# Optimization experiments

Hardware: AMD Instinct MI355X
Metric: run time of the kernel (lower is better)

Reference implementation:

```python
import jax, jax.numpy as jnp
import numpy as np

B, N, D = 32, 4096, 256      # batch, num input features, input dim
S, H, M = 11, 256, 512       # num_slots, slot_size, mlp_hidden_size
ITERS = 3
ATTN_EPS = 1e-8
LN_EPS = 1e-5


def layer_norm(x, scale, offset):
    mu = jnp.mean(x, axis=-1, keepdims=True)
    var = jnp.var(x, axis=-1, keepdims=True)
    return (x - mu) * scale * jax.lax.rsqrt(var + LN_EPS) + offset


def gru_unroll(updates, w_i, w_h, b):
    # haiku hk.GRU unrolled over axis 1 (time_major=False), zero initial state.
    # updates: [B, T, H]
    h0 = jnp.zeros((updates.shape[0], H), updates.dtype)
    def step(h, x):
        gx = jnp.matmul(x, w_i)                                    # [B, 3H]
        zr = jax.nn.sigmoid(gx[:, :2 * H] + jnp.matmul(h, w_h[:, :2 * H]) + b[:2 * H])
        z, r = zr[:, :H], zr[:, H:]
        a = jnp.tanh(gx[:, 2 * H:] + jnp.matmul(r * h, w_h[:, 2 * H:]) + b[2 * H:])
        h_new = (1.0 - z) * h + z * a
        return h_new, h_new
    _, outs = jax.lax.scan(step, h0, jnp.swapaxes(updates, 0, 1))
    return jnp.swapaxes(outs, 0, 1)                                # [B, T, H]


def setup_inputs():
    key = jax.random.key(0)
    k = jax.random.split(key, 16)
    def lin(kk, fan_in, fan_out):
        return jax.random.normal(kk, (fan_in, fan_out), jnp.float32) / np.sqrt(fan_in).astype(np.float32)
    return {
        "inputs": jax.random.normal(k[0], (B, N, D), jnp.float32),
        "slot_noise": jax.random.normal(k[1], (B, S, H), jnp.float32),
        "ln_in_scale": jnp.ones((D,), jnp.float32),
        "ln_in_offset": jnp.zeros((D,), jnp.float32),
        "ln_slots_scale": jnp.ones((H,), jnp.float32),
        "ln_slots_offset": jnp.zeros((H,), jnp.float32),
        "ln_mlp_scale": jnp.ones((H,), jnp.float32),
        "ln_mlp_offset": jnp.zeros((H,), jnp.float32),
        "slots_mu": jax.random.normal(k[2], (1, 1, H), jnp.float32) * 0.1,
        "slots_log_sigma": jax.random.normal(k[3], (1, 1, H), jnp.float32) * 0.1 - 1.0,
        "Wq": lin(k[4], H, H),
        "Wk": lin(k[5], D, H),
        "Wv": lin(k[6], D, H),
        "gru_wi": lin(k[7], H, 3 * H),
        "gru_wh": lin(k[8], H, 3 * H),
        "gru_b": jnp.zeros((3 * H,), jnp.float32),
        "mlp_w1": lin(k[9], H, M),
        "mlp_b1": jnp.zeros((M,), jnp.float32),
        "mlp_w2": lin(k[10], M, H),
        "mlp_b2": jnp.zeros((H,), jnp.float32),
    }


def reference(inputs, slot_noise, ln_in_scale, ln_in_offset, ln_slots_scale,
              ln_slots_offset, ln_mlp_scale, ln_mlp_offset, slots_mu,
              slots_log_sigma, Wq, Wk, Wv, gru_wi, gru_wh, gru_b,
              mlp_w1, mlp_b1, mlp_w2, mlp_b2):
    x = layer_norm(inputs, ln_in_scale, ln_in_offset)
    kf = jnp.matmul(x, Wk)                                          # [B, N, H]
    vf = jnp.matmul(x, Wv)                                          # [B, N, H]
    slots = slots_mu + jnp.exp(slots_log_sigma) * slot_noise        # [B, S, H]
    scale = H ** (-0.5)
    for _ in range(ITERS):
        q = jnp.matmul(layer_norm(slots, ln_slots_scale, ln_slots_offset), Wq) * scale
        attn_logits = jnp.einsum('bnh,bsh->bns', kf, q)             # [B, N, S]
        attn = jax.nn.softmax(attn_logits, axis=-1) + ATTN_EPS      # softmax over slots
        attn = attn / jnp.sum(attn, axis=-2, keepdims=True)         # normalize over inputs
        updates = jnp.einsum('bns,bnh->bsh', attn, vf)              # [B, S, H]
        slots = gru_unroll(updates, gru_wi, gru_wh, gru_b)          # GRU over slot axis
        mlp_in = layer_norm(slots, ln_mlp_scale, ln_mlp_offset)
        hid = jax.nn.relu(jnp.matmul(mlp_in, mlp_w1) + mlp_b1)
        slots = slots + jnp.matmul(hid, mlp_w2) + mlp_b2
    return slots
```

## Files before the change

### kernel.cpp

```cpp
#include <hip/hip_runtime.h>

typedef unsigned short u16;
typedef __bf16 bf16x8 __attribute__((ext_vector_type(8)));
typedef float  f32x4  __attribute__((ext_vector_type(4)));
typedef unsigned short u16x8 __attribute__((ext_vector_type(8)));

union U8cast { u16x8 u; bf16x8 b; };

#define NB 32
#define NN 4096
#define ND 256
#define NS 11
#define NH 256
#define NM 512

__device__ __forceinline__ u16 f2bf(float f) {
  unsigned u = __float_as_uint(f);
  u += 0x7FFF + ((u >> 16) & 1);
  return (u16)(u >> 16);
}
__device__ __forceinline__ float bf2f(u16 h) {
  return __uint_as_float(((unsigned)h) << 16);
}

__global__ void k_stats_ln(const float* __restrict__ x, const float* __restrict__ sc,
                           const float* __restrict__ of, u16* __restrict__ xbf) {
  int lane = threadIdx.x & 63;
  int wid  = threadIdx.x >> 6;
  int row  = blockIdx.x * 4 + wid;
  float4 v = *(const float4*)(x + (size_t)row * 256 + lane * 4);
  float s1 = v.x + v.y + v.z + v.w;
  float s2 = v.x*v.x + v.y*v.y + v.z*v.z + v.w*v.w;
#pragma unroll
  for (int off = 32; off; off >>= 1) { s1 += __shfl_xor(s1, off); s2 += __shfl_xor(s2, off); }
  float mu = s1 * (1.f/256.f);
  float rs = rsqrtf(s2 * (1.f/256.f) - mu*mu + 1e-5f);
  float4 s4 = *(const float4*)(sc + lane * 4);
  float4 o4 = *(const float4*)(of + lane * 4);
  ushort4 o;
  o.x = f2bf((v.x - mu) * (rs * s4.x) + o4.x);
  o.y = f2bf((v.y - mu) * (rs * s4.y) + o4.y);
  o.z = f2bf((v.z - mu) * (rs * s4.z) + o4.z);
  o.w = f2bf((v.w - mu) * (rs * s4.w) + o4.w);
  *(ushort4*)(xbf + (size_t)row * 256 + lane * 4) = o;
}

__global__ __launch_bounds__(256)
void k_cvt_w(const float* __restrict__ Wk, u16* __restrict__ wT) {
  __shared__ float Lt[64][65];
  int bx = blockIdx.x;
  int kt = bx & 3, ct = bx >> 2;
  int k0 = kt * 64, c0 = ct * 64;
  int t = threadIdx.x;
  int kr = t >> 2, part = t & 3;
  const float* sp = Wk + (size_t)(k0 + kr) * 256 + c0 + part * 16;
#pragma unroll
  for (int g = 0; g < 4; ++g) {
    float4 v = *(const float4*)(sp + g * 4);
    Lt[kr][part*16 + g*4 + 0] = v.x;
    Lt[kr][part*16 + g*4 + 1] = v.y;
    Lt[kr][part*16 + g*4 + 2] = v.z;
    Lt[kr][part*16 + g*4 + 3] = v.w;
  }
  __syncthreads();
  int cr = t >> 2;
  u16* wp = wT + (size_t)(c0 + cr) * 256 + k0 + part * 16;
#pragma unroll
  for (int g = 0; g < 2; ++g) {
    u16x8 o;
#pragma unroll
    for (int j = 0; j < 8; ++j) o[j] = f2bf(Lt[part*16 + g*8 + j][cr]);
    *(u16x8*)(wp + g * 8) = o;
  }
}

__global__ __launch_bounds__(256)
void k_mk(const float* __restrict__ Wq, const u16* __restrict__ wT,
          u16* __restrict__ Mb) {
  __shared__ float xn[256];
  __shared__ float part[8][256];
  int e = blockIdx.x, t = threadIdx.x;
  xn[t] = Wq[e*256 + t];
  __syncthreads();
  int tc = t & 31, kg = t >> 5;
  float a[8] = {};
#pragma unroll 8
  for (int kk = 0; kk < 32; ++kk) {
    int k = kg*32 + kk;
    float xv = xn[k];
    u16x8 wv = *(const u16x8*)(wT + k*256 + tc*8);
#pragma unroll
    for (int j = 0; j < 8; ++j) a[j] += xv * bf2f(wv[j]);
  }
  *(float4*)&part[kg][tc*8]     = make_float4(a[0], a[1], a[2], a[3]);
  *(float4*)&part[kg][tc*8 + 4] = make_float4(a[4], a[5], a[6], a[7]);
  __syncthreads();
  float s = 0.f;
#pragma unroll
  for (int g = 0; g < 8; ++g) s += part[g][t];
  Mb[e*256 + t] = f2bf(s);
}

__global__ __launch_bounds__(384)
void k_wvi(const float* __restrict__ Wv, const float* __restrict__ wi,
           u16* __restrict__ wvib) {
  __shared__ float xn[256];
  __shared__ float part[4][768];
  int d = blockIdx.x, t = threadIdx.x;
  if (t < 256) xn[t] = Wv[d*256 + t];
  __syncthreads();
  int tc = t % 96, kg = t / 96;
  float a[8] = {};
#pragma unroll 4
  for (int kk = 0; kk < 64; ++kk) {
    int k = kg*64 + kk;
    float xv = xn[k];
    float4 w0 = *(const float4*)(wi + (size_t)k*768 + tc*8);
    float4 w1 = *(const float4*)(wi + (size_t)k*768 + tc*8 + 4);
    a[0] += xv * w0.x; a[1] += xv * w0.y; a[2] += xv * w0.z; a[3] += xv * w0.w;
    a[4] += xv * w1.x; a[5] += xv * w1.y; a[6] += xv * w1.z; a[7] += xv * w1.w;
  }
  *(float4*)&part[kg][tc*8]     = make_float4(a[0], a[1], a[2], a[3]);
  *(float4*)&part[kg][tc*8 + 4] = make_float4(a[4], a[5], a[6], a[7]);
  __syncthreads();
#pragma unroll
  for (int c = t; c < 768; c += 384) {
    float s = part[0][c] + part[1][c] + part[2][c] + part[3][c];
    wvib[d*768 + c] = f2bf(s);
  }
}

__global__ void k_cvt_all(const float* __restrict__ wh, const float* __restrict__ w1,
                          const float* __restrict__ w2,
                          const float* __restrict__ noise, const float* __restrict__ smu,
                          const float* __restrict__ sls,
                          u16* __restrict__ whb, u16* __restrict__ w1b,
                          u16* __restrict__ w2b, float* __restrict__ slots) {
  int idx = blockIdx.x * 256 + threadIdx.x;
  if      (idx < 196608) whb[idx]          = f2bf(wh[idx]);
  else if (idx < 327680) w1b[idx - 196608] = f2bf(w1[idx - 196608]);
  else if (idx < 458752) w2b[idx - 327680] = f2bf(w2[idx - 327680]);
  else {
    int i = idx - 458752;
    int c = i & 255;
    slots[i] = smu[c] + expf(sls[c]) * noise[i];
  }
}

__global__ __launch_bounds__(256)
void k_q_ln(const float* __restrict__ slots, const float* __restrict__ sc,
            const float* __restrict__ of, const u16* __restrict__ Mb,
            float* __restrict__ qk2, float* __restrict__ updates,
            float* __restrict__ colsum) {
  __shared__ float xn[256];
  __shared__ float red[8];
  __shared__ float part[8][256];
  int row = blockIdx.x, t = threadIdx.x;
  float v = slots[row*256 + t];
  float s1 = v, s2 = v*v;
#pragma unroll
  for (int off = 32; off; off >>= 1) { s1 += __shfl_xor(s1, off); s2 += __shfl_xor(s2, off); }
  int w = t >> 6;
  if ((t & 63) == 0) { red[w*2] = s1; red[w*2+1] = s2; }
  __syncthreads();
  float a1 = red[0] + red[2] + red[4] + red[6];
  float a2 = red[1] + red[3] + red[5] + red[7];
  float mu = a1 * (1.f/256.f);
  float rs = rsqrtf(a2 * (1.f/256.f) - mu*mu + 1e-5f);
  xn[t] = (v - mu) * rs * sc[t] + of[t];
  updates[row*256 + t] = 0.f;
  if (t == 0) colsum[(row/11)*16 + (row%11)] = 0.f;
  __syncthreads();
  int tc = t & 31, kg = t >> 5;
  float a[8] = {};
#pragma unroll 8
  for (int kk = 0; kk < 32; ++kk) {
    int k = kg*32 + kk;
    float xv = xn[k];
    u16x8 wv = *(const u16x8*)(Mb + k*256 + tc*8);
#pragma unroll
    for (int j = 0; j < 8; ++j) a[j] += xv * bf2f(wv[j]);
  }
  *(float4*)&part[kg][tc*8]     = make_float4(a[0], a[1], a[2], a[3]);
  *(float4*)&part[kg][tc*8 + 4] = make_float4(a[4], a[5], a[6], a[7]);
  __syncthreads();
  float s = 0.f;
#pragma unroll
  for (int g = 0; g < 8; ++g) s += part[g][t];
  qk2[row*256 + t] = s * 0.0625f;
}

__global__ __launch_bounds__(256)
void k_attn_up(const u16* __restrict__ xbf, const float* __restrict__ qg,
               float* __restrict__ updates, float* __restrict__ colsum) {
  __shared__ __align__(16) u16 kfL[64][264];
  __shared__ __align__(16) u16 vfL[64][256];
  __shared__ __align__(16) u16 qTL[16][264];
  __shared__ __align__(16) u16 PTL[16][72];
  __shared__ float Lg[64][17];
  int t = threadIdx.x;
  int b = blockIdx.y;
  int nb0 = blockIdx.x * 256;
  int lane = t & 63, w = t >> 6;
  int fr = lane & 15, kq = lane >> 4;

#pragma unroll
  for (int i = t; i < 512; i += 256) {
    int s = i >> 5, k0 = (i & 31) * 8;
    u16x8 o;
    if (s < 11) {
      const float* qp = qg + (size_t)b*2816 + s*256 + k0;
#pragma unroll
      for (int j = 0; j < 8; ++j) o[j] = f2bf(qp[j]);
    } else {
#pragma unroll
      for (int j = 0; j < 8; ++j) o[j] = 0;
    }
    *(u16x8*)&qTL[s][k0] = o;
  }
  for (int i = t; i < 16*72; i += 256) ((u16*)PTL)[i] = 0;

  f32x4 accU[4] = {};
  float cs0 = 0.f, cs1 = 0.f, cs2 = 0.f;
  int rS = t >> 2, g4 = t & 3;

  for (int c = 0; c < 4; ++c) {
    int n0 = nb0 + c*64;
    __syncthreads();
    {
      int hc = (t & 31) * 8;
#pragma unroll
      for (int nr = 0; nr < 8; ++nr) {
        int n = nr*8 + (t >> 5);
        size_t base = ((size_t)b*4096 + n0 + n) * 256;
        u16x8 kvk = *(const u16x8*)(xbf + base + hc);
        *(u16x8*)&kfL[n][hc] = kvk;
        *(u16x8*)&vfL[n][hc ^ (((n >> 3) & 3) * 16)] = kvk;
      }
    }
    __syncthreads();
    {
      f32x4 aL = {};
#pragma unroll
      for (int kc = 0; kc < 256; kc += 32) {
        bf16x8 af = *(const bf16x8*)&kfL[w*16 + fr][kc + kq*8];
        bf16x8 bq = *(const bf16x8*)&qTL[fr][kc + kq*8];
        aL = __builtin_amdgcn_mfma_f32_16x16x32_bf16(af, bq, aL, 0, 0, 0);
      }
#pragma unroll
      for (int r = 0; r < 4; ++r)
        Lg[w*16 + kq*4 + r][fr] = aL[r];
    }
    __syncthreads();
    {
      float p0 = Lg[rS][g4];
      float p1 = Lg[rS][g4 + 4];
      float p2 = (g4 < 3) ? Lg[rS][g4 + 8] : -1e30f;
      float m = fmaxf(fmaxf(p0, p1), p2);
      m = fmaxf(m, __shfl_xor(m, 1));
      m = fmaxf(m, __shfl_xor(m, 2));
      p0 = __expf(p0 - m); p1 = __expf(p1 - m);
      p2 = (g4 < 3) ? __expf(p2 - m) : 0.f;
      float Z = p0 + p1 + p2;
      Z += __shfl_xor(Z, 1);
      Z += __shfl_xor(Z, 2);
      float iz = 1.f / Z;
      u16 b0 = f2bf(p0*iz + 1e-8f);
      u16 b1 = f2bf(p1*iz + 1e-8f);
      PTL[g4][rS]     = b0;  cs0 += bf2f(b0);
      PTL[g4 + 4][rS] = b1;  cs1 += bf2f(b1);
      if (g4 < 3) {
        u16 b2 = f2bf(p2*iz + 1e-8f);
        PTL[g4 + 8][rS] = b2;  cs2 += bf2f(b2);
      }
    }
    __syncthreads();
#pragma unroll
    for (int ht = 0; ht < 4; ++ht) {
      int h = w*64 + ht*16 + fr;
#pragma unroll
      for (int kc = 0; kc < 64; kc += 32) {
        bf16x8 aP = *(const bf16x8*)&PTL[fr][kc + kq*8];
        U8cast bv;
#pragma unroll
        for (int j = 0; j < 8; ++j) {
          int k = kc + kq*8 + j;
          bv.u[j] = vfL[k][h ^ (((k >> 3) & 3) * 16)];
        }
        accU[ht] = __builtin_amdgcn_mfma_f32_16x16x32_bf16(aP, bv.b, accU[ht], 0, 0, 0);
      }
    }
  }
#pragma unroll
  for (int ht = 0; ht < 4; ++ht) {
    int h = w*64 + ht*16 + fr;
#pragma unroll
    for (int r = 0; r < 4; ++r) {
      int s = kq*4 + r;
      if (s < 11)
        atomicAdd(&updates[((size_t)b*11 + s)*256 + h], accU[ht][r]);
    }
  }
  {
#pragma unroll
    for (int off = 4; off < 64; off <<= 1) {
      cs0 += __shfl_xor(cs0, off);
      cs1 += __shfl_xor(cs1, off);
      cs2 += __shfl_xor(cs2, off);
    }
    if (lane < 4) {
      atomicAdd(&colsum[b*16 + lane],     cs0);
      atomicAdd(&colsum[b*16 + lane + 4], cs1);
      if (lane < 3) atomicAdd(&colsum[b*16 + lane + 8], cs2);
    }
  }
}

__global__ __launch_bounds__(384)
void k_gx(const float* __restrict__ updates, const float* __restrict__ colsum,
          const u16* __restrict__ wvib, float* __restrict__ gx) {
  __shared__ float xn[256];
  __shared__ float part[4][768];
  int row = blockIdx.x, t = threadIdx.x;
  if (t < 256) {
    float inv = 1.f / colsum[(row/11)*16 + (row%11)];
    xn[t] = updates[row*256 + t] * inv;
  }
  __syncthreads();
  int tc = t % 96, kg = t / 96;
  float a[8] = {};
#pragma unroll 4
  for (int kk = 0; kk < 64; ++kk) {
    int k = kg*64 + kk;
    float xv = xn[k];
    u16x8 wv = *(const u16x8*)(wvib + k*768 + tc*8);
#pragma unroll
    for (int j = 0; j < 8; ++j) a[j] += xv * bf2f(wv[j]);
  }
  *(float4*)&part[kg][tc*8]     = make_float4(a[0], a[1], a[2], a[3]);
  *(float4*)&part[kg][tc*8 + 4] = make_float4(a[4], a[5], a[6], a[7]);
  __syncthreads();
#pragma unroll
  for (int c = t; c < 768; c += 384) {
    float s = part[0][c] + part[1][c] + part[2][c] + part[3][c];
    gx[row*768 + c] = s;
  }
}

__global__ __launch_bounds__(512)
void k_gru(const float* __restrict__ gx, const u16* __restrict__ whb,
           const float* __restrict__ gb, float* __restrict__ slots) {
  __shared__ float h[256], rh[256], zv[256];
  __shared__ float part[4096];
  int b = blockIdx.x, t = threadIdx.x;
  if (t < 256) h[t] = 0.f;
  __syncthreads();
  for (int step = 0; step < 11; ++step) {
    int row = b*11 + step;
    {
      int tc = t & 63, kg = t >> 6;
      float a[8] = {};
#pragma unroll 8
      for (int kk = 0; kk < 32; ++kk) {
        int k = kg*32 + kk;
        float xv = h[k];
        u16x8 wv = *(const u16x8*)(whb + k*768 + tc*8);
#pragma unroll
        for (int j = 0; j < 8; ++j) a[j] += xv * bf2f(wv[j]);
      }
      *(float4*)&part[kg*512 + tc*8]     = make_float4(a[0], a[1], a[2], a[3]);
      *(float4*)&part[kg*512 + tc*8 + 4] = make_float4(a[4], a[5], a[6], a[7]);
    }
    __syncthreads();
    {
      int c = t;
      float s = gx[row*768 + c] + gb[c];
#pragma unroll
      for (int g = 0; g < 8; ++g) s += part[g*512 + c];
      float sg = 1.f / (1.f + __expf(-s));
      if (c < 256) zv[c] = sg;
      else         rh[c - 256] = sg * h[c - 256];
    }
    __syncthreads();
    {
      int tc = t & 31, kg = t >> 5;
      float a[8] = {};
#pragma unroll 8
      for (int kk = 0; kk < 16; ++kk) {
        int k = kg*16 + kk;
        float xv = rh[k];
        u16x8 wv = *(const u16x8*)(whb + k*768 + 512 + tc*8);
#pragma unroll
        for (int j = 0; j < 8; ++j) a[j] += xv * bf2f(wv[j]);
      }
      *(float4*)&part[kg*256 + tc*8]     = make_float4(a[0], a[1], a[2], a[3]);
      *(float4*)&part[kg*256 + tc*8 + 4] = make_float4(a[4], a[5], a[6], a[7]);
    }
    __syncthreads();
    if (t < 256) {
      int c = t;
      float s = gx[row*768 + 512 + c] + gb[512 + c];
#pragma unroll
      for (int g = 0; g < 16; ++g) s += part[g*256 + c];
      float av = tanhf(s);
      float hn = (1.f - zv[c])*h[c] + zv[c]*av;
      h[c] = hn;
      slots[row*256 + c] = hn;
    }
    __syncthreads();
  }
}

__global__ __launch_bounds__(256)
void k_mlp(float* __restrict__ slots, const float* __restrict__ sc,
           const float* __restrict__ of, const u16* __restrict__ w1b,
           const float* __restrict__ b1, const u16* __restrict__ w2b,
           const float* __restrict__ b2, float* __restrict__ out2) {
  __shared__ float xn[256];
  __shared__ float hid[512];
  __shared__ float red[8];
  __shared__ float part[2048];
  int row = blockIdx.x, t = threadIdx.x;
  float v = slots[row*256 + t];
  float s1 = v, s2 = v*v;
#pragma unroll
  for (int off = 32; off; off >>= 1) { s1 += __shfl_xor(s1, off); s2 += __shfl_xor(s2, off); }
  int w = t >> 6;
  if ((t & 63) == 0) { red[w*2] = s1; red[w*2+1] = s2; }
  __syncthreads();
  float a1s = red[0] + red[2] + red[4] + red[6];
  float a2s = red[1] + red[3] + red[5] + red[7];
  float mu = a1s * (1.f/256.f);
  float rs = rsqrtf(a2s * (1.f/256.f) - mu*mu + 1e-5f);
  xn[t] = (v - mu) * rs * sc[t] + of[t];
  __syncthreads();
  {
    int tc = t & 63, kg = t >> 6;
    float a[8] = {};
#pragma unroll 4
    for (int kk = 0; kk < 64; ++kk) {
      int k = kg*64 + kk;
      float xv = xn[k];
      u16x8 wv = *(const u16x8*)(w1b + k*512 + tc*8);
#pragma unroll
      for (int j = 0; j < 8; ++j) a[j] += xv * bf2f(wv[j]);
    }
    *(float4*)&part[kg*512 + tc*8]     = make_float4(a[0], a[1], a[2], a[3]);
    *(float4*)&part[kg*512 + tc*8 + 4] = make_float4(a[4], a[5], a[6], a[7]);
  }
  __syncthreads();
#pragma unroll
  for (int c = t; c < 512; c += 256) {
    float s = b1[c];
#pragma unroll
    for (int g = 0; g < 4; ++g) s += part[g*512 + c];
    hid[c] = fmaxf(s, 0.f);
  }
  __syncthreads();
  {
    int tc = t & 31, kg = t >> 5;
    float a[8] = {};
#pragma unroll 4
    for (int kk = 0; kk < 64; ++kk) {
      int k = kg*64 + kk;
      float xv = hid[k];
      u16x8 wv = *(const u16x8*)(w2b + k*256 + tc*8);
#pragma unroll
      for (int j = 0; j < 8; ++j) a[j] += xv * bf2f(wv[j]);
    }
    *(float4*)&part[kg*256 + tc*8]     = make_float4(a[0], a[1], a[2], a[3]);
    *(float4*)&part[kg*256 + tc*8 + 4] = make_float4(a[4], a[5], a[6], a[7]);
  }
  __syncthreads();
  {
    float s = v + b2[t];
#pragma unroll
    for (int g = 0; g < 8; ++g) s += part[g*256 + t];
    slots[row*256 + t] = s;
    if (out2) out2[row*256 + t] = s;
  }
}

extern "C" void kernel_launch(void* const* d_in, const int* in_sizes, int n_in,
                              void* d_out, int out_size, void* d_ws, size_t ws_size,
                              hipStream_t stream) {
  (void)in_sizes; (void)n_in; (void)out_size; (void)ws_size;
  const float* inputs = (const float*)d_in[0];
  const float* noise  = (const float*)d_in[1];
  const float* lnin_s = (const float*)d_in[2];
  const float* lnin_o = (const float*)d_in[3];
  const float* lnsl_s = (const float*)d_in[4];
  const float* lnsl_o = (const float*)d_in[5];
  const float* lnml_s = (const float*)d_in[6];
  const float* lnml_o = (const float*)d_in[7];
  const float* smu    = (const float*)d_in[8];
  const float* sls    = (const float*)d_in[9];
  const float* Wq     = (const float*)d_in[10];
  const float* Wk     = (const float*)d_in[11];
  const float* Wv     = (const float*)d_in[12];
  const float* gwi    = (const float*)d_in[13];
  const float* gwh    = (const float*)d_in[14];
  const float* gb     = (const float*)d_in[15];
  const float* w1     = (const float*)d_in[16];
  const float* b1     = (const float*)d_in[17];
  const float* w2     = (const float*)d_in[18];
  const float* b2     = (const float*)d_in[19];

  char* ws = (char*)d_ws;
  u16*    wT      = (u16*)(ws + 134217728);
  float*  slots   = (float*)(ws + 139984896);
  float*  updates = (float*)(ws + 140345344);
  float*  gx      = (float*)(ws + 140705792);
  float*  qk2     = (float*)(ws + 140705792);
  float*  colsum  = (float*)(ws + 141787136);
  u16*    Mb      = (u16*)(ws + 141789184);
  u16*    wvib    = (u16*)(ws + 141920256);
  u16*    whb     = (u16*)(ws + 142313472);
  u16*    w1b     = (u16*)(ws + 142706688);
  u16*    w2b     = (u16*)(ws + 142968832);
  u16*    xbf     = (u16*)(ws + 143230976);

  k_stats_ln <<<32768, 256, 0, stream>>>(inputs, lnin_s, lnin_o, xbf);
  k_cvt_w    <<<16,    256, 0, stream>>>(Wk, wT);
  k_mk       <<<256,   256, 0, stream>>>(Wq, wT, Mb);
  k_wvi      <<<256,   384, 0, stream>>>(Wv, gwi, wvib);
  k_cvt_all  <<<2144,  256, 0, stream>>>(gwh, w1, w2, noise, smu, sls,
                                         whb, w1b, w2b, slots);

  for (int it = 0; it < 3; ++it) {
    k_q_ln    <<<352, 256, 0, stream>>>(slots, lnsl_s, lnsl_o, Mb, qk2, updates, colsum);
    k_attn_up <<<dim3(16, 32), 256, 0, stream>>>(xbf, qk2, updates, colsum);
    k_gx      <<<352, 384, 0, stream>>>(updates, colsum, wvib, gx);
    k_gru     <<<32,  512, 0, stream>>>(gx, whb, gb, slots);
    k_mlp     <<<352, 256, 0, stream>>>(slots, lnml_s, lnml_o, w1b, b1, w2b, b2,
                                        (it == 2) ? (float*)d_out : nullptr);
  }
}
```

Measured before the change: 547.5 us.

## Fuse next-iteration query projection into MLP kernel and keep GRU weights in registers

The per-iteration k_q_ln launch is removed. The MLP kernel now computes the slot layer norm and query projection for the next iteration, and it also zeroes the updates and colsum buffers; only the first k_q_ln remains before the loop. qk2 moves to its own workspace region so it no longer aliases gx. Separately, the GRU kernel loads its recurrent weight slices into registers once, instead of reloading them from global memory on each of the 11 steps, which raises register pressure under the new launch bounds.

```diff
diff --git a/kernel.cpp b/kernel.cpp
--- a/kernel.cpp
+++ b/kernel.cpp
@@ -347,29 +347,37 @@
   }
 }
 
-__global__ __launch_bounds__(512)
+__global__ __launch_bounds__(512, 2)
 void k_gru(const float* __restrict__ gx, const u16* __restrict__ whb,
            const float* __restrict__ gb, float* __restrict__ slots) {
   __shared__ float h[256], rh[256], zv[256];
   __shared__ float part[4096];
   int b = blockIdx.x, t = threadIdx.x;
+  int tc1 = t & 63, kg1 = t >> 6;
+  int tc2 = t & 31, kg2 = t >> 5;
+  u16x8 wA[32];
+#pragma unroll
+  for (int kk = 0; kk < 32; ++kk)
+    wA[kk] = *(const u16x8*)(whb + (size_t)(kg1*32 + kk)*768 + tc1*8);
+  u16x8 wB[16];
+#pragma unroll
+  for (int kk = 0; kk < 16; ++kk)
+    wB[kk] = *(const u16x8*)(whb + (size_t)(kg2*16 + kk)*768 + 512 + tc2*8);
   if (t < 256) h[t] = 0.f;
   __syncthreads();
   for (int step = 0; step < 11; ++step) {
     int row = b*11 + step;
     {
-      int tc = t & 63, kg = t >> 6;
       float a[8] = {};
-#pragma unroll 8
+#pragma unroll
       for (int kk = 0; kk < 32; ++kk) {
-        int k = kg*32 + kk;
-        float xv = h[k];
-        u16x8 wv = *(const u16x8*)(whb + k*768 + tc*8);
+        float xv = h[kg1*32 + kk];
+        u16x8 wv = wA[kk];
 #pragma unroll
         for (int j = 0; j < 8; ++j) a[j] += xv * bf2f(wv[j]);
       }
-      *(float4*)&part[kg*512 + tc*8]     = make_float4(a[0], a[1], a[2], a[3]);
-      *(float4*)&part[kg*512 + tc*8 + 4] = make_float4(a[4], a[5], a[6], a[7]);
+      *(float4*)&part[kg1*512 + tc1*8]     = make_float4(a[0], a[1], a[2], a[3]);
+      *(float4*)&part[kg1*512 + tc1*8 + 4] = make_float4(a[4], a[5], a[6], a[7]);
     }
     __syncthreads();
     {
@@ -383,18 +391,16 @@
     }
     __syncthreads();
     {
-      int tc = t & 31, kg = t >> 5;
       float a[8] = {};
-#pragma unroll 8
+#pragma unroll
       for (int kk = 0; kk < 16; ++kk) {
-        int k = kg*16 + kk;
-        float xv = rh[k];
-        u16x8 wv = *(const u16x8*)(whb + k*768 + 512 + tc*8);
+        float xv = rh[kg2*16 + kk];
+        u16x8 wv = wB[kk];
 #pragma unroll
         for (int j = 0; j < 8; ++j) a[j] += xv * bf2f(wv[j]);
       }
-      *(float4*)&part[kg*256 + tc*8]     = make_float4(a[0], a[1], a[2], a[3]);
-      *(float4*)&part[kg*256 + tc*8 + 4] = make_float4(a[4], a[5], a[6], a[7]);
+      *(float4*)&part[kg2*256 + tc2*8]     = make_float4(a[0], a[1], a[2], a[3]);
+      *(float4*)&part[kg2*256 + tc2*8 + 4] = make_float4(a[4], a[5], a[6], a[7]);
     }
     __syncthreads();
     if (t < 256) {
@@ -415,7 +421,11 @@
 void k_mlp(float* __restrict__ slots, const float* __restrict__ sc,
            const float* __restrict__ of, const u16* __restrict__ w1b,
            const float* __restrict__ b1, const u16* __restrict__ w2b,
-           const float* __restrict__ b2, float* __restrict__ out2) {
+           const float* __restrict__ b2,
+           const float* __restrict__ sls_, const float* __restrict__ slo,
+           const u16* __restrict__ Mb, float* __restrict__ qk2,
+           float* __restrict__ updates, float* __restrict__ colsum,
+           float* __restrict__ out2) {
   __shared__ float xn[256];
   __shared__ float hid[512];
   __shared__ float red[8];
@@ -472,12 +482,52 @@
     *(float4*)&part[kg*256 + tc*8 + 4] = make_float4(a[4], a[5], a[6], a[7]);
   }
   __syncthreads();
+  float snew;
   {
     float s = v + b2[t];
 #pragma unroll
     for (int g = 0; g < 8; ++g) s += part[g*256 + t];
-    slots[row*256 + t] = s;
-    if (out2) out2[row*256 + t] = s;
+    snew = s;
+    slots[row*256 + t] = snew;
+    if (out2) out2[row*256 + t] = snew;
+  }
+  updates[row*256 + t] = 0.f;
+  if (t == 0) colsum[(row/11)*16 + (row%11)] = 0.f;
+  if (!qk2) return;
+  float q1 = snew, q2 = snew*snew;
+#pragma unroll
+  for (int off = 32; off; off >>= 1) { q1 += __shfl_xor(q1, off); q2 += __shfl_xor(q2, off); }
+  __syncthreads();
+  if ((t & 63) == 0) { red[w*2] = q1; red[w*2+1] = q2; }
+  __syncthreads();
+  {
+    float b1v = red[0] + red[2] + red[4] + red[6];
+    float b2v = red[1] + red[3] + red[5] + red[7];
+    float mu2 = b1v * (1.f/256.f);
+    float rs2 = rsqrtf(b2v * (1.f/256.f) - mu2*mu2 + 1e-5f);
+    xn[t] = (snew - mu2) * rs2 * sls_[t] + slo[t];
+  }
+  __syncthreads();
+  {
+    int tc = t & 31, kg = t >> 5;
+    float a[8] = {};
+#pragma unroll 8
+    for (int kk = 0; kk < 32; ++kk) {
+      int k = kg*32 + kk;
+      float xv = xn[k];
+      u16x8 wv = *(const u16x8*)(Mb + k*256 + tc*8);
+#pragma unroll
+      for (int j = 0; j < 8; ++j) a[j] += xv * bf2f(wv[j]);
+    }
+    *(float4*)&part[kg*256 + tc*8]     = make_float4(a[0], a[1], a[2], a[3]);
+    *(float4*)&part[kg*256 + tc*8 + 4] = make_float4(a[4], a[5], a[6], a[7]);
+  }
+  __syncthreads();
+  {
+    float s = 0.f;
+#pragma unroll
+    for (int g = 0; g < 8; ++g) s += part[g*256 + t];
+    qk2[row*256 + t] = s * 0.0625f;
   }
 }
 
@@ -508,10 +558,10 @@
 
   char* ws = (char*)d_ws;
   u16*    wT      = (u16*)(ws + 134217728);
+  float*  qk2     = (float*)(ws + 135000064);
   float*  slots   = (float*)(ws + 139984896);
   float*  updates = (float*)(ws + 140345344);
   float*  gx      = (float*)(ws + 140705792);
-  float*  qk2     = (float*)(ws + 140705792);
   float*  colsum  = (float*)(ws + 141787136);
   u16*    Mb      = (u16*)(ws + 141789184);
   u16*    wvib    = (u16*)(ws + 141920256);
@@ -526,13 +576,16 @@
   k_wvi      <<<256,   384, 0, stream>>>(Wv, gwi, wvib);
   k_cvt_all  <<<2144,  256, 0, stream>>>(gwh, w1, w2, noise, smu, sls,
                                          whb, w1b, w2b, slots);
+  k_q_ln     <<<352,   256, 0, stream>>>(slots, lnsl_s, lnsl_o, Mb, qk2, updates, colsum);
 
   for (int it = 0; it < 3; ++it) {
-    k_q_ln    <<<352, 256, 0, stream>>>(slots, lnsl_s, lnsl_o, Mb, qk2, updates, colsum);
     k_attn_up <<<dim3(16, 32), 256, 0, stream>>>(xbf, qk2, updates, colsum);
     k_gx      <<<352, 384, 0, stream>>>(updates, colsum, wvib, gx);
     k_gru     <<<32,  512, 0, stream>>>(gx, whb, gb, slots);
     k_mlp     <<<352, 256, 0, stream>>>(slots, lnml_s, lnml_o, w1b, b1, w2b, b2,
+                                        lnsl_s, lnsl_o, Mb,
+                                        (it < 2) ? qk2 : nullptr,
+                                        updates, colsum,
                                         (it == 2) ? (float*)d_out : nullptr);
   }
 }
```

Measured after the change: 864.5 us. 57.9% more time.
